# Optimization experiments

Hardware: AMD Instinct MI355X
Metric: run time of the kernel (lower is better)

The kernel has to match this reference:

```python
import jax, jax.numpy as jnp
import numpy as np

H = 8          # num_heads
C = 32         # dim_head
S = 64         # num_slices
D = H * C      # hidden_dim


def setup_inputs() -> dict:
    key = jax.random.key(0)
    ks = jax.random.split(key, 8)
    B, N = 1, 262144
    std = 0.02
    return {
        "x": jax.random.normal(ks[0], (B, N, D), jnp.float32),
        "W_fx": jax.random.normal(ks[1], (D, D), jnp.float32) * std,
        "b_fx": jnp.zeros((D,), jnp.float32),
        "W_x": jax.random.normal(ks[2], (D, D), jnp.float32) * std,
        "b_x": jnp.zeros((D,), jnp.float32),
        "W_slice": jax.random.normal(ks[3], (C, S), jnp.float32) * std,
        "b_slice": jnp.zeros((S,), jnp.float32),
        "W_qkv": jax.random.normal(ks[4], (C, 3 * C), jnp.float32) * std,
        "W_proj": jax.random.normal(ks[5], (D, D), jnp.float32) * std,
        "b_proj": jnp.zeros((D,), jnp.float32),
        "temperature": jnp.full((1, H, 1, 1), 0.5, jnp.float32),
    }


def reference(x, W_fx, b_fx, W_x, b_x, W_slice, b_slice, W_qkv, W_proj, b_proj, temperature):
    B, N, _ = x.shape
    # project and split heads: [B, H, N, C]
    fx_mid = (x @ W_fx + b_fx).reshape(B, N, H, C).transpose(0, 2, 1, 3)
    x_mid = (x @ W_x + b_x).reshape(B, N, H, C).transpose(0, 2, 1, 3)

    # soft routing of tokens to slices: [B, H, N, S]
    slice_logits = (x_mid @ W_slice + b_slice) / temperature
    slice_weights = jax.nn.softmax(slice_logits, axis=-1)

    # weighted pooling into slice tokens: [B, H, S, C]
    slice_norm = slice_weights.sum(axis=2)[..., None]  # [B, H, S, 1]
    slice_tokens = jnp.einsum('bhnc,bhns->bhsc', fx_mid, slice_weights) / (slice_norm + 1e-5)

    # SDPA over the tiny slice dim
    qkv = slice_tokens @ W_qkv  # [B, H, S, 3C]
    q, k, v = jnp.split(qkv, 3, axis=-1)
    scores = jnp.einsum('bhsc,bhtc->bhst', q, k) / jnp.sqrt(jnp.float32(C))
    attn = jax.nn.softmax(scores, axis=-1)
    out_slice = jnp.einsum('bhst,bhtc->bhsc', attn, v)

    # scatter back to tokens: [B, H, N, C] -> [B, N, D]
    out_x = jnp.einsum('bhsc,bhns->bhnc', out_slice, slice_weights)
    out_x = out_x.transpose(0, 2, 1, 3).reshape(B, N, D)
    return out_x @ W_proj + b_proj
```

## Files before the change

### kernel.cpp

```cpp
#include <hip/hip_runtime.h>
#include <math.h>

#define NTOK 262144
#define DIM  256
#define NH   8
#define CH   32
#define NS   64

typedef __attribute__((ext_vector_type(8))) short short8v;
typedef __attribute__((ext_vector_type(4))) float float4v;

constexpr size_t OFF_MID   = 0;
constexpr size_t OFF_WCT   = 268435456;
constexpr size_t OFF_WPT   = OFF_WCT + 262144;
constexpr size_t OFF_POOLP = OFF_WPT + 131072;
constexpr size_t OFF_NORMP = OFF_POOLP + 33554432;
constexpr size_t OFF_SSUM  = OFF_NORMP + 1048576;
constexpr size_t OFF_NSUM  = OFF_SSUM + 65536;
constexpr size_t OFF_OSL   = OFF_NSUM + 2048;

#define KA_LDS_B 81920
#define KB_LDS_F (18432 + 2048 + 64)
#define KD_LDS_B 139648

__device__ __forceinline__ unsigned short f2bf(float f) {
    unsigned u = __float_as_uint(f);
    unsigned r = (u + 0x7fffu + ((u >> 16) & 1u)) >> 16;
    return (unsigned short)r;
}
__device__ __forceinline__ float bf2f(unsigned short u) {
    return __uint_as_float(((unsigned)u) << 16);
}

__device__ __forceinline__ void compute_w_bf(const unsigned short* __restrict__ xm,
                                             const float* __restrict__ wsl,
                                             const float* __restrict__ bsl,
                                             float invT, float* lg)
{
    float xv[32];
    #pragma unroll
    for (int q = 0; q < 4; ++q) {
        const uint4 u = *(const uint4*)(xm + q*8);
        const unsigned vals[4] = {u.x, u.y, u.z, u.w};
        #pragma unroll
        for (int j = 0; j < 4; ++j) {
            xv[q*8 + j*2 + 0] = __uint_as_float(vals[j] << 16);
            xv[q*8 + j*2 + 1] = __uint_as_float(vals[j] & 0xffff0000u);
        }
    }
    #pragma unroll
    for (int s = 0; s < 64; ++s) lg[s] = bsl[s];
    #pragma unroll
    for (int c = 0; c < 32; ++c) {
        const float xvj = xv[c];
        const float* wr = wsl + c*64;
        #pragma unroll
        for (int s4 = 0; s4 < 16; ++s4) {
            const float4 w4 = *(const float4*)(wr + s4*4);
            lg[s4*4+0] = fmaf(xvj, w4.x, lg[s4*4+0]);
            lg[s4*4+1] = fmaf(xvj, w4.y, lg[s4*4+1]);
            lg[s4*4+2] = fmaf(xvj, w4.z, lg[s4*4+2]);
            lg[s4*4+3] = fmaf(xvj, w4.w, lg[s4*4+3]);
        }
    }
    float m = -1e30f;
    #pragma unroll
    for (int s = 0; s < 64; ++s) { lg[s] *= invT; m = fmaxf(m, lg[s]); }
    float sum = 0.f;
    #pragma unroll
    for (int s = 0; s < 64; ++s) { lg[s] = expf(lg[s] - m); sum += lg[s]; }
    const float r = 1.0f / sum;
    #pragma unroll
    for (int s = 0; s < 64; ++s) lg[s] *= r;
}

__device__ __forceinline__ void scat_acc(const float* __restrict__ orow, float wv, float* ox)
{
    #pragma unroll
    for (int c4 = 0; c4 < 8; ++c4) {
        const float4 o4 = *(const float4*)(orow + c4*4);
        ox[c4*4+0] = fmaf(wv, o4.x, ox[c4*4+0]);
        ox[c4*4+1] = fmaf(wv, o4.y, ox[c4*4+1]);
        ox[c4*4+2] = fmaf(wv, o4.z, ox[c4*4+2]);
        ox[c4*4+3] = fmaf(wv, o4.w, ox[c4*4+3]);
    }
}

__global__ void __launch_bounds__(512) tk_w(
    const float* __restrict__ Wfx, const float* __restrict__ Wx,
    const float* __restrict__ Wproj,
    unsigned short* __restrict__ WcatT, unsigned short* __restrict__ WprojT)
{
    const int t = threadIdx.x, b = blockIdx.x;
    const int rl = t >> 4, q = t & 15;
    if (b < 16) {
        const int r = b*32 + rl;
        #pragma unroll
        for (int j = 0; j < 16; ++j) {
            const int k = q*16 + j;
            const float v = (r < 256) ? Wfx[(size_t)k*256 + r] : Wx[(size_t)k*256 + (r-256)];
            WcatT[(size_t)r*256 + k] = f2bf(v);
        }
    } else {
        const int r = (b-16)*32 + rl;
        #pragma unroll
        for (int j = 0; j < 16; ++j) {
            const int k = q*16 + j;
            WprojT[(size_t)r*256 + k] = f2bf(Wproj[(size_t)k*256 + r]);
        }
    }
}

__global__ void __launch_bounds__(512, 2) tk_a(
    const float* __restrict__ x,
    const unsigned short* __restrict__ WcatT,
    const float* __restrict__ bfx, const float* __restrict__ bx,
    unsigned short* __restrict__ midp)
{
    extern __shared__ char smem[];
    char* astage = smem;
    char* bstage = smem + 16384;

    const int t = threadIdx.x;
    const int l = t & 63, w = t >> 6;
    const int wm = w >> 2, wn = w & 3;
    const int m0 = blockIdx.x * 128;

    float4v acc[4][8];
    #pragma unroll
    for (int mr = 0; mr < 4; ++mr)
        #pragma unroll
        for (int nr = 0; nr < 8; ++nr)
            acc[mr][nr] = (float4v){0.f, 0.f, 0.f, 0.f};

    const int ar = t >> 2, aq = t & 3;

    for (int c = 0; c < 4; ++c) {
        {
            const float* xr = x + (size_t)(m0 + ar)*256 + c*64 + aq*16;
            const float4 f0 = *(const float4*)(xr + 0);
            const float4 f1 = *(const float4*)(xr + 4);
            const float4 f2 = *(const float4*)(xr + 8);
            const float4 f3 = *(const float4*)(xr + 12);
            short8v v0, v1;
            v0[0]=(short)f2bf(f0.x); v0[1]=(short)f2bf(f0.y); v0[2]=(short)f2bf(f0.z); v0[3]=(short)f2bf(f0.w);
            v0[4]=(short)f2bf(f1.x); v0[5]=(short)f2bf(f1.y); v0[6]=(short)f2bf(f1.z); v0[7]=(short)f2bf(f1.w);
            v1[0]=(short)f2bf(f2.x); v1[1]=(short)f2bf(f2.y); v1[2]=(short)f2bf(f2.z); v1[3]=(short)f2bf(f2.w);
            v1[4]=(short)f2bf(f3.x); v1[5]=(short)f2bf(f3.y); v1[6]=(short)f2bf(f3.z); v1[7]=(short)f2bf(f3.w);
            const int ob = ar*128 + aq*32;
            *(short8v*)(astage + ((ob     ) ^ ((ar & 7) << 4))) = v0;
            *(short8v*)(astage + ((ob + 16) ^ ((ar & 7) << 4))) = v1;
        }
        {
            const int n = t;
            #pragma unroll
            for (int j = 0; j < 8; ++j) {
                const uint4 u = *(const uint4*)(WcatT + (size_t)n*256 + c*64 + j*8);
                *(uint4*)(bstage + ((n*128 + j*16) ^ ((n & 7) << 4))) = u;
            }
        }
        __syncthreads();
        #pragma unroll
        for (int ks = 0; ks < 2; ++ks) {
            short8v a[4], b[8];
            const int kof = (ks*32 + (l >> 4)*8) * 2;
            #pragma unroll
            for (int mr = 0; mr < 4; ++mr) {
                const int m = wm*64 + mr*16 + (l & 15);
                a[mr] = *(const short8v*)(astage + ((m*128 + kof) ^ ((m & 7) << 4)));
            }
            #pragma unroll
            for (int nr = 0; nr < 8; ++nr) {
                const int n = wn*128 + nr*16 + (l & 15);
                b[nr] = *(const short8v*)(bstage + ((n*128 + kof) ^ ((n & 7) << 4)));
            }
            #pragma unroll
            for (int mr = 0; mr < 4; ++mr)
                #pragma unroll
                for (int nr = 0; nr < 8; ++nr)
                    acc[mr][nr] = __builtin_amdgcn_mfma_f32_16x16x32_bf16(
                        a[mr], b[nr], acc[mr][nr], 0, 0, 0);
        }
        __syncthreads();
    }

    float bias_n[8];
    #pragma unroll
    for (int nr = 0; nr < 8; ++nr) {
        const int col = wn*128 + nr*16 + (l & 15);
        bias_n[nr] = (col < 256) ? bfx[col] : bx[col - 256];
    }
    #pragma unroll
    for (int mr = 0; mr < 4; ++mr) {
        #pragma unroll
        for (int reg = 0; reg < 4; ++reg) {
            const int row = m0 + wm*64 + mr*16 + (l >> 4)*4 + reg;
            #pragma unroll
            for (int nr = 0; nr < 8; ++nr) {
                const int col = wn*128 + nr*16 + (l & 15);
                midp[(size_t)row*512 + col] = f2bf(acc[mr][nr][reg] + bias_n[nr]);
            }
        }
    }
}

__global__ void __launch_bounds__(512, 2) tk_b(
    const unsigned short* __restrict__ midp,
    const float* __restrict__ Wslc, const float* __restrict__ bslc,
    const float* __restrict__ temp,
    float* __restrict__ poolp, float* __restrict__ normp)
{
    extern __shared__ float sm[];
    float* wls = sm;
    float* wsl = sm + 18432;
    float* bsl = wsl + 2048;

    const int t   = threadIdx.x;
    const int blk = blockIdx.x;

    for (int i = t; i < 2048; i += 512) wsl[i] = Wslc[i];
    if (t < 64) bsl[t] = bslc[t];
    __syncthreads();

    const int cg = t & 255, ihalf = t >> 8;
    const int hP = cg >> 5;
    const int cP = cg & 31;
    const int iL = t >> 3,   hL = t & 7;
    const int hN = t >> 6;
    const int sN = (t >> 1) & 31, iqN = t & 1;

    float pool[64];
    #pragma unroll
    for (int s = 0; s < 64; ++s) pool[s] = 0.f;
    float nacc0 = 0.f, nacc1 = 0.f;

    const float invT = 1.0f / temp[hL];

    for (int tl = 0; tl < 8; ++tl) {
        const int n0 = blk*512 + tl*64;

        float afx[32];
        #pragma unroll
        for (int ii = 0; ii < 32; ++ii)
            afx[ii] = bf2f(midp[(size_t)(n0 + ihalf*32 + ii)*512 + cg]);

        float lg[64];
        compute_w_bf(midp + (size_t)(n0 + iL)*512 + 256 + hL*32, wsl, bsl, invT, lg);

        #pragma unroll
        for (int sh = 0; sh < 2; ++sh) {
            float* wrow = wls + t*36;
            #pragma unroll
            for (int sl = 0; sl < 32; sl += 2)
                *(float2*)(wrow + sl) = make_float2(lg[sh*32+sl], lg[sh*32+sl+1]);
            __syncthreads();
            #pragma unroll
            for (int ii = 0; ii < 32; ++ii) {
                const float fxv = afx[ii];
                const float* wr2 = wls + ((ihalf*32+ii)*8 + hP)*36;
                #pragma unroll
                for (int s4 = 0; s4 < 8; ++s4) {
                    const float4 w4 = *(const float4*)(wr2 + s4*4);
                    pool[sh*32+s4*4+0] = fmaf(fxv, w4.x, pool[sh*32+s4*4+0]);
                    pool[sh*32+s4*4+1] = fmaf(fxv, w4.y, pool[sh*32+s4*4+1]);
                    pool[sh*32+s4*4+2] = fmaf(fxv, w4.z, pool[sh*32+s4*4+2]);
                    pool[sh*32+s4*4+3] = fmaf(fxv, w4.w, pool[sh*32+s4*4+3]);
                }
            }
            {
                float na = 0.f;
                #pragma unroll
                for (int ii = 0; ii < 32; ++ii)
                    na += wls[((iqN*32+ii)*8 + hN)*36 + sN];
                if (sh == 0) nacc0 += na; else nacc1 += na;
            }
            __syncthreads();
        }
    }

    if (ihalf == 1) {
        float* buf = wls + cg*65;
        #pragma unroll
        for (int s = 0; s < 64; ++s) buf[s] = pool[s];
    }
    if (iqN == 1) {
        wls[16640 + (hN*32+sN)*2 + 0] = nacc0;
        wls[16640 + (hN*32+sN)*2 + 1] = nacc1;
    }
    __syncthreads();
    if (ihalf == 0) {
        const float* buf = wls + cg*65;
        float* dst = poolp + (size_t)blk*(NH*NS*CH) + (size_t)hP*(NS*CH) + cP;
        #pragma unroll
        for (int s = 0; s < 64; ++s) dst[(size_t)s*CH] = pool[s] + buf[s];
    }
    if (iqN == 0) {
        const float v0 = nacc0 + wls[16640 + (hN*32+sN)*2 + 0];
        const float v1 = nacc1 + wls[16640 + (hN*32+sN)*2 + 1];
        normp[(size_t)blk*512 + hN*64 + sN]      = v0;
        normp[(size_t)blk*512 + hN*64 + 32 + sN] = v1;
    }
}

__global__ void __launch_bounds__(256) tk_2a(
    const float* __restrict__ poolp, const float* __restrict__ normp,
    float* __restrict__ ssum, float* __restrict__ nsum)
{
    const int idx = blockIdx.x*256 + threadIdx.x;
    if (idx < 16384) {
        float a0=0.f,a1=0.f,a2=0.f,a3=0.f;
        for (int b = 0; b < 512; b += 4) {
            a0 += poolp[(size_t)(b+0)*16384 + idx];
            a1 += poolp[(size_t)(b+1)*16384 + idx];
            a2 += poolp[(size_t)(b+2)*16384 + idx];
            a3 += poolp[(size_t)(b+3)*16384 + idx];
        }
        ssum[idx] = (a0+a1)+(a2+a3);
    } else if (idx < 16896) {
        const int j = idx - 16384;
        float a0=0.f,a1=0.f,a2=0.f,a3=0.f;
        for (int b = 0; b < 512; b += 4) {
            a0 += normp[(size_t)(b+0)*512 + j];
            a1 += normp[(size_t)(b+1)*512 + j];
            a2 += normp[(size_t)(b+2)*512 + j];
            a3 += normp[(size_t)(b+3)*512 + j];
        }
        nsum[j] = (a0+a1)+(a2+a3);
    }
}

__global__ void __launch_bounds__(64) tk_2b(
    const float* __restrict__ ssum, const float* __restrict__ nsum,
    const float* __restrict__ Wqkv, float* __restrict__ osl)
{
    __shared__ float ks[64*36];
    __shared__ float vs[64*36];
    const int h = blockIdx.x;
    const int s = threadIdx.x;

    const float inv = 1.0f / (nsum[h*64 + s] + 1e-5f);
    const float* st = ssum + h*2048 + s*32;

    float q[32], kk[32], vv[32];
    #pragma unroll
    for (int j = 0; j < 32; ++j) { q[j]=0.f; kk[j]=0.f; vv[j]=0.f; }
    for (int c = 0; c < 32; ++c) {
        const float sv = st[c] * inv;
        const float* wr = Wqkv + c*96;
        #pragma unroll
        for (int j4 = 0; j4 < 8; ++j4) {
            const float4 a = *(const float4*)(wr + j4*4);
            q[j4*4+0]=fmaf(sv,a.x,q[j4*4+0]); q[j4*4+1]=fmaf(sv,a.y,q[j4*4+1]);
            q[j4*4+2]=fmaf(sv,a.z,q[j4*4+2]); q[j4*4+3]=fmaf(sv,a.w,q[j4*4+3]);
            const float4 b = *(const float4*)(wr + 32 + j4*4);
            kk[j4*4+0]=fmaf(sv,b.x,kk[j4*4+0]); kk[j4*4+1]=fmaf(sv,b.y,kk[j4*4+1]);
            kk[j4*4+2]=fmaf(sv,b.z,kk[j4*4+2]); kk[j4*4+3]=fmaf(sv,b.w,kk[j4*4+3]);
            const float4 d = *(const float4*)(wr + 64 + j4*4);
            vv[j4*4+0]=fmaf(sv,d.x,vv[j4*4+0]); vv[j4*4+1]=fmaf(sv,d.y,vv[j4*4+1]);
            vv[j4*4+2]=fmaf(sv,d.z,vv[j4*4+2]); vv[j4*4+3]=fmaf(sv,d.w,vv[j4*4+3]);
        }
    }
    #pragma unroll
    for (int c = 0; c < 32; ++c) { ks[s*36+c] = kk[c]; vs[s*36+c] = vv[c]; }
    __syncthreads();

    const float scale = 1.0f / sqrtf(32.0f);
    float sc[64];
    #pragma unroll
    for (int tt = 0; tt < 64; ++tt) {
        float acc = 0.f;
        #pragma unroll
        for (int c4 = 0; c4 < 8; ++c4) {
            const float4 k4 = *(const float4*)(ks + tt*36 + c4*4);
            acc = fmaf(q[c4*4+0],k4.x,acc); acc = fmaf(q[c4*4+1],k4.y,acc);
            acc = fmaf(q[c4*4+2],k4.z,acc); acc = fmaf(q[c4*4+3],k4.w,acc);
        }
        sc[tt] = acc * scale;
    }
    float m = -1e30f;
    #pragma unroll
    for (int tt = 0; tt < 64; ++tt) m = fmaxf(m, sc[tt]);
    float sum = 0.f;
    #pragma unroll
    for (int tt = 0; tt < 64; ++tt) { sc[tt] = expf(sc[tt]-m); sum += sc[tt]; }
    const float r = 1.0f / sum;
    #pragma unroll
    for (int tt = 0; tt < 64; ++tt) sc[tt] *= r;

    float o[32];
    #pragma unroll
    for (int c = 0; c < 32; ++c) o[c] = 0.f;
    #pragma unroll
    for (int tt = 0; tt < 64; ++tt) {
        const float av = sc[tt];
        #pragma unroll
        for (int c4 = 0; c4 < 8; ++c4) {
            const float4 v4 = *(const float4*)(vs + tt*36 + c4*4);
            o[c4*4+0]=fmaf(av,v4.x,o[c4*4+0]); o[c4*4+1]=fmaf(av,v4.y,o[c4*4+1]);
            o[c4*4+2]=fmaf(av,v4.z,o[c4*4+2]); o[c4*4+3]=fmaf(av,v4.w,o[c4*4+3]);
        }
    }
    float* dst = osl + h*2048 + s*32;
    #pragma unroll
    for (int c = 0; c < 32; ++c) dst[c] = o[c];
}

__global__ void __launch_bounds__(512, 2) tk_d(
    const unsigned short* __restrict__ midp,
    const float* __restrict__ Wslc, const float* __restrict__ bslc,
    const float* __restrict__ temp,
    const float* __restrict__ oslg,
    const unsigned short* __restrict__ WprojT,
    const float* __restrict__ bp,
    float* __restrict__ out)
{
    extern __shared__ float sm[];
    float* oslds = sm;
    float* wsl   = sm + 16416;
    float* bsl   = wsl + 2048;
    char*  atile = (char*)(bsl + 64);
    char*  btile = atile + 32768;

    const int t  = threadIdx.x;
    const int l  = t & 63, wv = t >> 6;
    const int n0 = blockIdx.x * 64;

    for (int i = t; i < 2048; i += 512) wsl[i] = Wslc[i];
    if (t < 64) bsl[t] = bslc[t];
    #pragma unroll
    for (int rr = 0; rr < 32; ++rr) {
        const int idx = rr*512 + t;
        oslds[(idx >> 11)*2052 + (idx & 2047)] = oslg[idx];
    }
    __syncthreads();

    const int iL = t >> 3, hL = t & 7;
    const float invT = 1.0f / temp[hL];
    float lg[64];
    compute_w_bf(midp + (size_t)(n0 + iL)*512 + 256 + hL*32, wsl, bsl, invT, lg);

    float ox[32];
    #pragma unroll
    for (int c = 0; c < 32; ++c) ox[c] = 0.f;
    const float* obase = oslds + hL*2052;
    #pragma unroll
    for (int s = 0; s < 64; ++s)
        scat_acc(obase + s*32, lg[s], ox);

    #pragma unroll
    for (int c0 = 0; c0 < 32; c0 += 8) {
        short8v v;
        #pragma unroll
        for (int j = 0; j < 8; ++j) v[j] = (short)f2bf(ox[c0+j]);
        const int ob = iL*512 + (hL*32 + c0)*2;
        *(short8v*)(atile + (ob ^ ((iL & 7) << 4))) = v;
    }
    __syncthreads();

    float4v acc[4][2];
    #pragma unroll
    for (int mr = 0; mr < 4; ++mr)
        #pragma unroll
        for (int nr = 0; nr < 2; ++nr)
            acc[mr][nr] = (float4v){0.f, 0.f, 0.f, 0.f};

    const int bn = t >> 1, bh = t & 1;
    for (int c = 0; c < 4; ++c) {
        #pragma unroll
        for (int j = 0; j < 4; ++j) {
            const uint4 u = *(const uint4*)(WprojT + (size_t)bn*256 + c*64 + bh*32 + j*8);
            const int kk = bh*32 + j*8;
            *(uint4*)(btile + ((bn*128 + kk*2) ^ ((bn & 7) << 4))) = u;
        }
        __syncthreads();
        #pragma unroll
        for (int ks = 0; ks < 2; ++ks) {
            short8v a[4], b[2];
            const int kof = (ks*32 + (l >> 4)*8) * 2;
            #pragma unroll
            for (int mr = 0; mr < 4; ++mr) {
                const int m = mr*16 + (l & 15);
                a[mr] = *(const short8v*)(atile + ((m*512 + c*128 + kof) ^ ((m & 7) << 4)));
            }
            #pragma unroll
            for (int nr = 0; nr < 2; ++nr) {
                const int n = wv*32 + nr*16 + (l & 15);
                b[nr] = *(const short8v*)(btile + ((n*128 + kof) ^ ((n & 7) << 4)));
            }
            #pragma unroll
            for (int mr = 0; mr < 4; ++mr)
                #pragma unroll
                for (int nr = 0; nr < 2; ++nr)
                    acc[mr][nr] = __builtin_amdgcn_mfma_f32_16x16x32_bf16(
                        a[mr], b[nr], acc[mr][nr], 0, 0, 0);
        }
        __syncthreads();
    }

    float bias_n[2];
    #pragma unroll
    for (int nr = 0; nr < 2; ++nr) bias_n[nr] = bp[wv*32 + nr*16 + (l & 15)];
    #pragma unroll
    for (int mr = 0; mr < 4; ++mr) {
        #pragma unroll
        for (int reg = 0; reg < 4; ++reg) {
            const int row = n0 + mr*16 + (l >> 4)*4 + reg;
            #pragma unroll
            for (int nr = 0; nr < 2; ++nr) {
                const int col = wv*32 + nr*16 + (l & 15);
                out[(size_t)row*256 + col] = acc[mr][nr][reg] + bias_n[nr];
            }
        }
    }
}

extern "C" void kernel_launch(void* const* d_in, const int* in_sizes, int n_in,
                              void* d_out, int out_size, void* d_ws, size_t ws_size,
                              hipStream_t stream)
{
    const float* x     = (const float*)d_in[0];
    const float* Wfx   = (const float*)d_in[1];
    const float* bfx   = (const float*)d_in[2];
    const float* Wx    = (const float*)d_in[3];
    const float* bx    = (const float*)d_in[4];
    const float* Wslc  = (const float*)d_in[5];
    const float* bslc  = (const float*)d_in[6];
    const float* Wqkv  = (const float*)d_in[7];
    const float* Wproj = (const float*)d_in[8];
    const float* bproj = (const float*)d_in[9];
    const float* temp  = (const float*)d_in[10];

    char* wsb = (char*)d_ws;
    unsigned short* midp   = (unsigned short*)(wsb + OFF_MID);
    unsigned short* WcatT  = (unsigned short*)(wsb + OFF_WCT);
    unsigned short* WprojT = (unsigned short*)(wsb + OFF_WPT);
    float* poolp = (float*)(wsb + OFF_POOLP);
    float* normp = (float*)(wsb + OFF_NORMP);
    float* ssum  = (float*)(wsb + OFF_SSUM);
    float* nsum  = (float*)(wsb + OFF_NSUM);
    float* osl   = (float*)(wsb + OFF_OSL);
    float* out   = (float*)d_out;

    (void)hipFuncSetAttribute((const void*)tk_a, hipFuncAttributeMaxDynamicSharedMemorySize, KA_LDS_B);
    (void)hipFuncSetAttribute((const void*)tk_b, hipFuncAttributeMaxDynamicSharedMemorySize, KB_LDS_F*4);
    (void)hipFuncSetAttribute((const void*)tk_d, hipFuncAttributeMaxDynamicSharedMemorySize, KD_LDS_B);

    tk_w<<<24, 512, 0, stream>>>(Wfx, Wx, Wproj, WcatT, WprojT);
    tk_a<<<2048, 512, KA_LDS_B, stream>>>(x, WcatT, bfx, bx, midp);
    tk_b<<<512, 512, KB_LDS_F*4, stream>>>(midp, Wslc, bslc, temp, poolp, normp);
    tk_2a<<<66, 256, 0, stream>>>(poolp, normp, ssum, nsum);
    tk_2b<<<8, 64, 0, stream>>>(ssum, nsum, Wqkv, osl);
    tk_d<<<4096, 512, KD_LDS_B, stream>>>(midp, Wslc, bslc, temp, osl, WprojT, bproj, out);
}
```

Before: 2.098 ms.

## Split mid buffer into transposed fx and token-major xm layouts

The GEMM epilogue now writes the fx half of the projection transposed (channel-major, token contiguous) with 4-wide packed stores, and the x half into its own token-major buffer. The pooling kernel then reads fx with 16-byte vector loads along tokens instead of strided scalar loads. The slice-weight LDS row stride also drops from 36 to 34 floats, with float2 reads in place of float4. The transposed store scatters across widely separated rows, and the new LDS stride may change bank conflicts.

After: 2.234 ms. 6.5% more time.

```diff
diff --git a/kernel.cpp b/kernel.cpp
--- a/kernel.cpp
+++ b/kernel.cpp
@@ -8,9 +8,11 @@
 #define NS   64
 
 typedef __attribute__((ext_vector_type(8))) short short8v;
+typedef __attribute__((ext_vector_type(4))) short short4v;
 typedef __attribute__((ext_vector_type(4))) float float4v;
 
-constexpr size_t OFF_MID   = 0;
+constexpr size_t OFF_MIDFX = 0;
+constexpr size_t OFF_MIDXM = 134217728;
 constexpr size_t OFF_WCT   = 268435456;
 constexpr size_t OFF_WPT   = OFF_WCT + 262144;
 constexpr size_t OFF_POOLP = OFF_WPT + 131072;
@@ -20,7 +22,7 @@
 constexpr size_t OFF_OSL   = OFF_NSUM + 2048;
 
 #define KA_LDS_B 81920
-#define KB_LDS_F (18432 + 2048 + 64)
+#define KB_LDS_F (17408 + 2048 + 64)
 #define KD_LDS_B 139648
 
 __device__ __forceinline__ unsigned short f2bf(float f) {
@@ -115,7 +117,7 @@
     const float* __restrict__ x,
     const unsigned short* __restrict__ WcatT,
     const float* __restrict__ bfx, const float* __restrict__ bx,
-    unsigned short* __restrict__ midp)
+    unsigned short* __restrict__ midfx, unsigned short* __restrict__ midxm)
 {
     extern __shared__ char smem[];
     char* astage = smem;
@@ -184,35 +186,54 @@
         __syncthreads();
     }
 
-    float bias_n[8];
-    #pragma unroll
-    for (int nr = 0; nr < 8; ++nr) {
-        const int col = wn*128 + nr*16 + (l & 15);
-        bias_n[nr] = (col < 256) ? bfx[col] : bx[col - 256];
-    }
-    #pragma unroll
-    for (int mr = 0; mr < 4; ++mr) {
-        #pragma unroll
-        for (int reg = 0; reg < 4; ++reg) {
-            const int row = m0 + wm*64 + mr*16 + (l >> 4)*4 + reg;
+    if (wn < 2) {
+        float bias_n[8];
+        #pragma unroll
+        for (int nr = 0; nr < 8; ++nr) bias_n[nr] = bfx[wn*128 + nr*16 + (l & 15)];
+        #pragma unroll
+        for (int mr = 0; mr < 4; ++mr) {
+            const int row0 = m0 + wm*64 + mr*16 + (l >> 4)*4;
             #pragma unroll
             for (int nr = 0; nr < 8; ++nr) {
                 const int col = wn*128 + nr*16 + (l & 15);
-                midp[(size_t)row*512 + col] = f2bf(acc[mr][nr][reg] + bias_n[nr]);
+                const float bv = bias_n[nr];
+                short4v p;
+                p[0] = (short)f2bf(acc[mr][nr][0] + bv);
+                p[1] = (short)f2bf(acc[mr][nr][1] + bv);
+                p[2] = (short)f2bf(acc[mr][nr][2] + bv);
+                p[3] = (short)f2bf(acc[mr][nr][3] + bv);
+                *(short4v*)(midfx + (size_t)col*NTOK + row0) = p;
+            }
+        }
+    } else {
+        float bias_n[8];
+        #pragma unroll
+        for (int nr = 0; nr < 8; ++nr) bias_n[nr] = bx[(wn-2)*128 + nr*16 + (l & 15)];
+        #pragma unroll
+        for (int mr = 0; mr < 4; ++mr) {
+            #pragma unroll
+            for (int reg = 0; reg < 4; ++reg) {
+                const int row = m0 + wm*64 + mr*16 + (l >> 4)*4 + reg;
+                #pragma unroll
+                for (int nr = 0; nr < 8; ++nr) {
+                    const int col = (wn-2)*128 + nr*16 + (l & 15);
+                    midxm[(size_t)row*256 + col] = f2bf(acc[mr][nr][reg] + bias_n[nr]);
+                }
             }
         }
     }
 }
 
 __global__ void __launch_bounds__(512, 2) tk_b(
-    const unsigned short* __restrict__ midp,
+    const unsigned short* __restrict__ midfx,
+    const unsigned short* __restrict__ midxm,
     const float* __restrict__ Wslc, const float* __restrict__ bslc,
     const float* __restrict__ temp,
     float* __restrict__ poolp, float* __restrict__ normp)
 {
     extern __shared__ float sm[];
     float* wls = sm;
-    float* wsl = sm + 18432;
+    float* wsl = sm + 17408;
     float* bsl = wsl + 2048;
 
     const int t   = threadIdx.x;
@@ -240,16 +261,26 @@
         const int n0 = blk*512 + tl*64;
 
         float afx[32];
-        #pragma unroll
-        for (int ii = 0; ii < 32; ++ii)
-            afx[ii] = bf2f(midp[(size_t)(n0 + ihalf*32 + ii)*512 + cg]);
+        {
+            const unsigned short* fr = midfx + (size_t)cg*NTOK + n0 + ihalf*32;
+            #pragma unroll
+            for (int q = 0; q < 4; ++q) {
+                const uint4 u = *(const uint4*)(fr + q*8);
+                const unsigned vals[4] = {u.x, u.y, u.z, u.w};
+                #pragma unroll
+                for (int j = 0; j < 4; ++j) {
+                    afx[q*8 + j*2 + 0] = __uint_as_float(vals[j] << 16);
+                    afx[q*8 + j*2 + 1] = __uint_as_float(vals[j] & 0xffff0000u);
+                }
+            }
+        }
 
         float lg[64];
-        compute_w_bf(midp + (size_t)(n0 + iL)*512 + 256 + hL*32, wsl, bsl, invT, lg);
+        compute_w_bf(midxm + (size_t)(n0 + iL)*256 + hL*32, wsl, bsl, invT, lg);
 
         #pragma unroll
         for (int sh = 0; sh < 2; ++sh) {
-            float* wrow = wls + t*36;
+            float* wrow = wls + t*34;
             #pragma unroll
             for (int sl = 0; sl < 32; sl += 2)
                 *(float2*)(wrow + sl) = make_float2(lg[sh*32+sl], lg[sh*32+sl+1]);
@@ -257,21 +288,19 @@
             #pragma unroll
             for (int ii = 0; ii < 32; ++ii) {
                 const float fxv = afx[ii];
-                const float* wr2 = wls + ((ihalf*32+ii)*8 + hP)*36;
+                const float* wr2 = wls + ((ihalf*32+ii)*8 + hP)*34;
                 #pragma unroll
-                for (int s4 = 0; s4 < 8; ++s4) {
-                    const float4 w4 = *(const float4*)(wr2 + s4*4);
-                    pool[sh*32+s4*4+0] = fmaf(fxv, w4.x, pool[sh*32+s4*4+0]);
-                    pool[sh*32+s4*4+1] = fmaf(fxv, w4.y, pool[sh*32+s4*4+1]);
-                    pool[sh*32+s4*4+2] = fmaf(fxv, w4.z, pool[sh*32+s4*4+2]);
-                    pool[sh*32+s4*4+3] = fmaf(fxv, w4.w, pool[sh*32+s4*4+3]);
+                for (int s8 = 0; s8 < 16; ++s8) {
+                    const float2 w2 = *(const float2*)(wr2 + s8*2);
+                    pool[sh*32+s8*2+0] = fmaf(fxv, w2.x, pool[sh*32+s8*2+0]);
+                    pool[sh*32+s8*2+1] = fmaf(fxv, w2.y, pool[sh*32+s8*2+1]);
                 }
             }
             {
                 float na = 0.f;
                 #pragma unroll
                 for (int ii = 0; ii < 32; ++ii)
-                    na += wls[((iqN*32+ii)*8 + hN)*36 + sN];
+                    na += wls[((iqN*32+ii)*8 + hN)*34 + sN];
                 if (sh == 0) nacc0 += na; else nacc1 += na;
             }
             __syncthreads();
@@ -406,7 +435,7 @@
 }
 
 __global__ void __launch_bounds__(512, 2) tk_d(
-    const unsigned short* __restrict__ midp,
+    const unsigned short* __restrict__ midxm,
     const float* __restrict__ Wslc, const float* __restrict__ bslc,
     const float* __restrict__ temp,
     const float* __restrict__ oslg,
@@ -437,7 +466,7 @@
     const int iL = t >> 3, hL = t & 7;
     const float invT = 1.0f / temp[hL];
     float lg[64];
-    compute_w_bf(midp + (size_t)(n0 + iL)*512 + 256 + hL*32, wsl, bsl, invT, lg);
+    compute_w_bf(midxm + (size_t)(n0 + iL)*256 + hL*32, wsl, bsl, invT, lg);
 
     float ox[32];
     #pragma unroll
@@ -531,7 +560,8 @@
     const float* temp  = (const float*)d_in[10];
 
     char* wsb = (char*)d_ws;
-    unsigned short* midp   = (unsigned short*)(wsb + OFF_MID);
+    unsigned short* midfx  = (unsigned short*)(wsb + OFF_MIDFX);
+    unsigned short* midxm  = (unsigned short*)(wsb + OFF_MIDXM);
     unsigned short* WcatT  = (unsigned short*)(wsb + OFF_WCT);
     unsigned short* WprojT = (unsigned short*)(wsb + OFF_WPT);
     float* poolp = (float*)(wsb + OFF_POOLP);
@@ -546,9 +576,9 @@
     (void)hipFuncSetAttribute((const void*)tk_d, hipFuncAttributeMaxDynamicSharedMemorySize, KD_LDS_B);
 
     tk_w<<<24, 512, 0, stream>>>(Wfx, Wx, Wproj, WcatT, WprojT);
-    tk_a<<<2048, 512, KA_LDS_B, stream>>>(x, WcatT, bfx, bx, midp);
-    tk_b<<<512, 512, KB_LDS_F*4, stream>>>(midp, Wslc, bslc, temp, poolp, normp);
+    tk_a<<<2048, 512, KA_LDS_B, stream>>>(x, WcatT, bfx, bx, midfx, midxm);
+    tk_b<<<512, 512, KB_LDS_F*4, stream>>>(midfx, midxm, Wslc, bslc, temp, poolp, normp);
     tk_2a<<<66, 256, 0, stream>>>(poolp, normp, ssum, nsum);
     tk_2b<<<8, 64, 0, stream>>>(ssum, nsum, Wqkv, osl);
-    tk_d<<<4096, 512, KD_LDS_B, stream>>>(midp, Wslc, bslc, temp, osl, WprojT, bproj, out);
-}
+    tk_d<<<4096, 512, KD_LDS_B, stream>>>(midxm, Wslc, bslc, temp, osl, WprojT, bproj, out);
+}
```

## Fold slice outputs into projection weights and run scatter+proj as one MFMA GEMM

Applied to the files above, without the earlier changes.

Precomputes, per head, out_slice @ W_proj rows (a 512x256 bf16 matrix) in the tiny attention kernel. The final kernel then multiplies the bf16 slice weights (64 tokens x 512 head-slices) by this matrix with MFMA, instead of doing a scalar-FMA scatter of 64 slices x 32 channels per token followed by a K=256 GEMM. It also double-buffers the B-tile loads across the eight K chunks. The GEMM K doubles to 512 and tk_2b does more serial work, and the slice weights are rounded to bf16, which risks precision.

Result: faster. 1.951 ms (-7.0%).

```diff
diff --git a/kernel.cpp b/kernel.cpp
--- a/kernel.cpp
+++ b/kernel.cpp
@@ -12,16 +12,15 @@
 
 constexpr size_t OFF_MID   = 0;
 constexpr size_t OFF_WCT   = 268435456;
-constexpr size_t OFF_WPT   = OFF_WCT + 262144;
-constexpr size_t OFF_POOLP = OFF_WPT + 131072;
+constexpr size_t OFF_POOLP = OFF_WCT + 262144;
 constexpr size_t OFF_NORMP = OFF_POOLP + 33554432;
 constexpr size_t OFF_SSUM  = OFF_NORMP + 1048576;
 constexpr size_t OFF_NSUM  = OFF_SSUM + 65536;
-constexpr size_t OFF_OSL   = OFF_NSUM + 2048;
+constexpr size_t OFF_OPT   = OFF_NSUM + 2048;
 
 #define KA_LDS_B 81920
 #define KB_LDS_F (18432 + 2048 + 64)
-#define KD_LDS_B 139648
+#define KD_LDS_B (65536 + 65536 + 8192 + 256)
 
 __device__ __forceinline__ unsigned short f2bf(float f) {
     unsigned u = __float_as_uint(f);
@@ -74,40 +73,18 @@
     for (int s = 0; s < 64; ++s) lg[s] *= r;
 }
 
-__device__ __forceinline__ void scat_acc(const float* __restrict__ orow, float wv, float* ox)
-{
-    #pragma unroll
-    for (int c4 = 0; c4 < 8; ++c4) {
-        const float4 o4 = *(const float4*)(orow + c4*4);
-        ox[c4*4+0] = fmaf(wv, o4.x, ox[c4*4+0]);
-        ox[c4*4+1] = fmaf(wv, o4.y, ox[c4*4+1]);
-        ox[c4*4+2] = fmaf(wv, o4.z, ox[c4*4+2]);
-        ox[c4*4+3] = fmaf(wv, o4.w, ox[c4*4+3]);
-    }
-}
-
 __global__ void __launch_bounds__(512) tk_w(
     const float* __restrict__ Wfx, const float* __restrict__ Wx,
-    const float* __restrict__ Wproj,
-    unsigned short* __restrict__ WcatT, unsigned short* __restrict__ WprojT)
+    unsigned short* __restrict__ WcatT)
 {
     const int t = threadIdx.x, b = blockIdx.x;
     const int rl = t >> 4, q = t & 15;
-    if (b < 16) {
-        const int r = b*32 + rl;
-        #pragma unroll
-        for (int j = 0; j < 16; ++j) {
-            const int k = q*16 + j;
-            const float v = (r < 256) ? Wfx[(size_t)k*256 + r] : Wx[(size_t)k*256 + (r-256)];
-            WcatT[(size_t)r*256 + k] = f2bf(v);
-        }
-    } else {
-        const int r = (b-16)*32 + rl;
-        #pragma unroll
-        for (int j = 0; j < 16; ++j) {
-            const int k = q*16 + j;
-            WprojT[(size_t)r*256 + k] = f2bf(Wproj[(size_t)k*256 + r]);
-        }
+    const int r = b*32 + rl;
+    #pragma unroll
+    for (int j = 0; j < 16; ++j) {
+        const int k = q*16 + j;
+        const float v = (r < 256) ? Wfx[(size_t)k*256 + r] : Wx[(size_t)k*256 + (r-256)];
+        WcatT[(size_t)r*256 + k] = f2bf(v);
     }
 }
 
@@ -331,7 +308,8 @@
 
 __global__ void __launch_bounds__(64) tk_2b(
     const float* __restrict__ ssum, const float* __restrict__ nsum,
-    const float* __restrict__ Wqkv, float* __restrict__ osl)
+    const float* __restrict__ Wqkv, const float* __restrict__ Wproj,
+    unsigned short* __restrict__ opt)
 {
     __shared__ float ks[64*36];
     __shared__ float vs[64*36];
@@ -400,37 +378,59 @@
             o[c4*4+2]=fmaf(av,v4.z,o[c4*4+2]); o[c4*4+3]=fmaf(av,v4.w,o[c4*4+3]);
         }
     }
-    float* dst = osl + h*2048 + s*32;
-    #pragma unroll
-    for (int c = 0; c < 32; ++c) dst[c] = o[c];
+
+    for (int pc = 0; pc < 4; ++pc) {
+        float op[64];
+        #pragma unroll
+        for (int j = 0; j < 64; ++j) op[j] = 0.f;
+        for (int c = 0; c < 32; ++c) {
+            const float oc = o[c];
+            const float* wr = Wproj + (size_t)(h*32 + c)*256 + pc*64;
+            #pragma unroll
+            for (int j4 = 0; j4 < 16; ++j4) {
+                const float4 w4 = *(const float4*)(wr + j4*4);
+                op[j4*4+0] = fmaf(oc, w4.x, op[j4*4+0]);
+                op[j4*4+1] = fmaf(oc, w4.y, op[j4*4+1]);
+                op[j4*4+2] = fmaf(oc, w4.z, op[j4*4+2]);
+                op[j4*4+3] = fmaf(oc, w4.w, op[j4*4+3]);
+            }
+        }
+        #pragma unroll
+        for (int j = 0; j < 64; ++j)
+            opt[(size_t)(pc*64 + j)*512 + h*64 + s] = f2bf(op[j]);
+    }
 }
 
 __global__ void __launch_bounds__(512, 2) tk_d(
     const unsigned short* __restrict__ midp,
     const float* __restrict__ Wslc, const float* __restrict__ bslc,
     const float* __restrict__ temp,
-    const float* __restrict__ oslg,
-    const unsigned short* __restrict__ WprojT,
+    const unsigned short* __restrict__ optg,
     const float* __restrict__ bp,
     float* __restrict__ out)
 {
-    extern __shared__ float sm[];
-    float* oslds = sm;
-    float* wsl   = sm + 16416;
-    float* bsl   = wsl + 2048;
-    char*  atile = (char*)(bsl + 64);
-    char*  btile = atile + 32768;
-
-    const int t  = threadIdx.x;
-    const int l  = t & 63, wv = t >> 6;
+    extern __shared__ char smem[];
+    char*  alds = smem;
+    char*  bst  = smem + 65536;
+    float* wsl  = (float*)(smem + 131072);
+    float* bsl  = wsl + 2048;
+
+    const int t = threadIdx.x;
+    const int l = t & 63, wv = t >> 6;
     const int n0 = blockIdx.x * 64;
 
     for (int i = t; i < 2048; i += 512) wsl[i] = Wslc[i];
     if (t < 64) bsl[t] = bslc[t];
-    #pragma unroll
-    for (int rr = 0; rr < 32; ++rr) {
-        const int idx = rr*512 + t;
-        oslds[(idx >> 11)*2052 + (idx & 2047)] = oslg[idx];
+
+    const int sp = t >> 1, shalf = t & 1;
+    {
+        const unsigned short* src = optg + (size_t)sp*512 + shalf*32;
+        #pragma unroll
+        for (int j = 0; j < 4; ++j) {
+            const uint4 u = *(const uint4*)(src + j*8);
+            const int off = shalf*64 + j*16;
+            *(uint4*)(bst + sp*128 + (off ^ ((sp & 7) << 4))) = u;
+        }
     }
     __syncthreads();
 
@@ -439,21 +439,13 @@
     float lg[64];
     compute_w_bf(midp + (size_t)(n0 + iL)*512 + 256 + hL*32, wsl, bsl, invT, lg);
 
-    float ox[32];
-    #pragma unroll
-    for (int c = 0; c < 32; ++c) ox[c] = 0.f;
-    const float* obase = oslds + hL*2052;
-    #pragma unroll
-    for (int s = 0; s < 64; ++s)
-        scat_acc(obase + s*32, lg[s], ox);
-
-    #pragma unroll
-    for (int c0 = 0; c0 < 32; c0 += 8) {
+    #pragma unroll
+    for (int j = 0; j < 8; ++j) {
         short8v v;
         #pragma unroll
-        for (int j = 0; j < 8; ++j) v[j] = (short)f2bf(ox[c0+j]);
-        const int ob = iL*512 + (hL*32 + c0)*2;
-        *(short8v*)(atile + (ob ^ ((iL & 7) << 4))) = v;
+        for (int e = 0; e < 8; ++e) v[e] = (short)f2bf(lg[j*8+e]);
+        const int off = hL*128 + j*16;
+        *(short8v*)(alds + iL*1024 + (off ^ ((iL & 7) << 4))) = v;
     }
     __syncthreads();
 
@@ -464,28 +456,33 @@
         for (int nr = 0; nr < 2; ++nr)
             acc[mr][nr] = (float4v){0.f, 0.f, 0.f, 0.f};
 
-    const int bn = t >> 1, bh = t & 1;
-    for (int c = 0; c < 4; ++c) {
-        #pragma unroll
-        for (int j = 0; j < 4; ++j) {
-            const uint4 u = *(const uint4*)(WprojT + (size_t)bn*256 + c*64 + bh*32 + j*8);
-            const int kk = bh*32 + j*8;
-            *(uint4*)(btile + ((bn*128 + kk*2) ^ ((bn & 7) << 4))) = u;
-        }
-        __syncthreads();
-        #pragma unroll
-        for (int ks = 0; ks < 2; ++ks) {
+    int buf = 0;
+    for (int kc = 0; kc < 8; ++kc) {
+        if (kc < 7) {
+            const unsigned short* src = optg + (size_t)sp*512 + (kc+1)*64 + shalf*32;
+            char* bdst = bst + (buf^1)*32768;
+            #pragma unroll
+            for (int j = 0; j < 4; ++j) {
+                const uint4 u = *(const uint4*)(src + j*8);
+                const int off = shalf*64 + j*16;
+                *(uint4*)(bdst + sp*128 + (off ^ ((sp & 7) << 4))) = u;
+            }
+        }
+        const char* bcur = bst + buf*32768;
+        #pragma unroll
+        for (int ksi = 0; ksi < 2; ++ksi) {
             short8v a[4], b[2];
-            const int kof = (ks*32 + (l >> 4)*8) * 2;
             #pragma unroll
             for (int mr = 0; mr < 4; ++mr) {
-                const int m = mr*16 + (l & 15);
-                a[mr] = *(const short8v*)(atile + ((m*512 + c*128 + kof) ^ ((m & 7) << 4)));
+                const int row = mr*16 + (l & 15);
+                const int off = kc*128 + ksi*64 + (l >> 4)*16;
+                a[mr] = *(const short8v*)(alds + row*1024 + (off ^ ((row & 7) << 4)));
             }
             #pragma unroll
             for (int nr = 0; nr < 2; ++nr) {
                 const int n = wv*32 + nr*16 + (l & 15);
-                b[nr] = *(const short8v*)(btile + ((n*128 + kof) ^ ((n & 7) << 4)));
+                const int off = ksi*64 + (l >> 4)*16;
+                b[nr] = *(const short8v*)(bcur + n*128 + (off ^ ((n & 7) << 4)));
             }
             #pragma unroll
             for (int mr = 0; mr < 4; ++mr)
@@ -495,6 +492,7 @@
                         a[mr], b[nr], acc[mr][nr], 0, 0, 0);
         }
         __syncthreads();
+        buf ^= 1;
     }
 
     float bias_n[2];
@@ -531,24 +529,23 @@
     const float* temp  = (const float*)d_in[10];
 
     char* wsb = (char*)d_ws;
-    unsigned short* midp   = (unsigned short*)(wsb + OFF_MID);
-    unsigned short* WcatT  = (unsigned short*)(wsb + OFF_WCT);
-    unsigned short* WprojT = (unsigned short*)(wsb + OFF_WPT);
+    unsigned short* midp  = (unsigned short*)(wsb + OFF_MID);
+    unsigned short* WcatT = (unsigned short*)(wsb + OFF_WCT);
     float* poolp = (float*)(wsb + OFF_POOLP);
     float* normp = (float*)(wsb + OFF_NORMP);
     float* ssum  = (float*)(wsb + OFF_SSUM);
     float* nsum  = (float*)(wsb + OFF_NSUM);
-    float* osl   = (float*)(wsb + OFF_OSL);
+    unsigned short* opt = (unsigned short*)(wsb + OFF_OPT);
     float* out   = (float*)d_out;
 
     (void)hipFuncSetAttribute((const void*)tk_a, hipFuncAttributeMaxDynamicSharedMemorySize, KA_LDS_B);
     (void)hipFuncSetAttribute((const void*)tk_b, hipFuncAttributeMaxDynamicSharedMemorySize, KB_LDS_F*4);
     (void)hipFuncSetAttribute((const void*)tk_d, hipFuncAttributeMaxDynamicSharedMemorySize, KD_LDS_B);
 
-    tk_w<<<24, 512, 0, stream>>>(Wfx, Wx, Wproj, WcatT, WprojT);
+    tk_w<<<16, 512, 0, stream>>>(Wfx, Wx, WcatT);
     tk_a<<<2048, 512, KA_LDS_B, stream>>>(x, WcatT, bfx, bx, midp);
     tk_b<<<512, 512, KB_LDS_F*4, stream>>>(midp, Wslc, bslc, temp, poolp, normp);
     tk_2a<<<66, 256, 0, stream>>>(poolp, normp, ssum, nsum);
-    tk_2b<<<8, 64, 0, stream>>>(ssum, nsum, Wqkv, osl);
-    tk_d<<<4096, 512, KD_LDS_B, stream>>>(midp, Wslc, bslc, temp, osl, WprojT, bproj, out);
-}
+    tk_2b<<<8, 64, 0, stream>>>(ssum, nsum, Wqkv, Wproj, opt);
+    tk_d<<<4096, 512, KD_LDS_B, stream>>>(midp, Wslc, bslc, temp, opt, bproj, out);
+}
```
